# Performance work log

Hardware: AMD Instinct MI355X
Metric: run time of the kernel (lower is better)

The kernel has to match this reference:

```python
import jax, jax.numpy as jnp
import numpy as np

MARGIN = 0.1
B, D, NUM_CLASSES = 512, 128, 64


def _pairwise_sq_dist(e):
    # squared pairwise distances with clamp + off-diagonal masking,
    # matching pairwise_distance_torch (NOTE: no sqrt in the original).
    sq = jnp.sum(e * e, axis=-1)                       # [B]
    d = sq[:, None] + sq[None, :] - 2.0 * (e @ e.T)    # [B, B]
    d = jnp.maximum(d, 0.0)
    d = d * (d > 0.0).astype(jnp.float32)              # error_mask step
    n = e.shape[0]
    return d * (1.0 - jnp.eye(n, dtype=jnp.float32))   # zero diagonal


def setup_inputs() -> dict:
    key = jax.random.key(0)
    k1, k2 = jax.random.split(key)
    emb = jax.random.normal(k1, (B, D), dtype=jnp.float32)
    emb = emb / jnp.linalg.norm(emb, axis=-1, keepdims=True)  # l2-normalized per docstring
    labels = jax.random.randint(k2, (B,), 0, NUM_CLASSES, dtype=jnp.int64 if jax.config.read('jax_enable_x64') else jnp.int32)
    return {"embeddings": emb, "labels": labels}


def reference(embeddings, labels):
    e = embeddings.astype(jnp.float32)
    pdist = _pairwise_sq_dist(e)                       # [B, B]
    n = labels.shape[0]
    adj = labels[:, None] == labels[None, :]           # [B, B] bool
    adj_not = ~adj

    # Tiled mining tensor, expressed as [i, j, k] where j = anchor,
    # k = negative candidate, i = positive candidate.
    # mask3[i, j, k] = (label[j] != label[k]) & (d(j,k) > d(j,i))
    mask3 = (adj_not[None, :, :] & (pdist[None, :, :] > pdist.T[:, :, None])).astype(jnp.float32)

    # masked min over negatives k (min-over-mask via row-max shift trick, as in torch code)
    row_max = jnp.max(pdist, axis=1, keepdims=True)    # [B, 1] per anchor j
    mm = jnp.min((pdist[None, :, :] - row_max[None, :, :]) * mask3, axis=2) + row_max[None, :, 0]  # [i, j]
    negatives_outside = mm.T                           # [anchor j, positive i]
    mask_final = (jnp.sum(mask3, axis=2) > 0.0).T      # [j, i]: semi-hard negative exists

    # fallback: hardest (largest) negative per anchor
    row_min = jnp.min(pdist, axis=1, keepdims=True)    # [B, 1]
    anf = adj_not.astype(jnp.float32)
    masked_max = jnp.max((pdist - row_min) * anf, axis=1, keepdims=True) + row_min  # [B, 1]
    negatives_inside = jnp.broadcast_to(masked_max, (n, n))

    semi_hard_negatives = jnp.where(mask_final, negatives_outside, negatives_inside)
    loss_mat = MARGIN + pdist - semi_hard_negatives

    mask_positives = adj.astype(jnp.float32) - jnp.eye(n, dtype=jnp.float32)
    num_positives = jnp.sum(mask_positives)
    triplet_loss = jnp.sum(jnp.maximum(loss_mat * mask_positives, 0.0)) / num_positives
    return triplet_loss.astype(embeddings.dtype)
```

## Files before the change

kernel.cpp:

```cpp
#include <hip/hip_runtime.h>
#include <cfloat>


constexpr int   BN       = 512;
constexpr int   DD       = 128;
constexpr float MARGIN_F = 0.1f;
constexpr int   NBLK     = BN / 2;

template <int CTRL>
__device__ inline float dppAdd(float v) {
    int x = __builtin_amdgcn_update_dpp(__float_as_int(v), __float_as_int(v),
                                        CTRL, 0xF, 0xF, false);
    return v + __int_as_float(x);
}
template <int CTRL>
__device__ inline float dppMin(float v) {
    int x = __builtin_amdgcn_update_dpp(__float_as_int(v), __float_as_int(v),
                                        CTRL, 0xF, 0xF, false);
    return fminf(v, __int_as_float(x));
}
template <int CTRL>
__device__ inline float dppMax(float v) {
    int x = __builtin_amdgcn_update_dpp(__float_as_int(v), __float_as_int(v),
                                        CTRL, 0xF, 0xF, false);
    return fmaxf(v, __int_as_float(x));
}
constexpr int DPP_XOR1 = 0xB1;
constexpr int DPP_XOR2 = 0x4E;
constexpr int DPP_ROR4 = 0x124;
constexpr int DPP_ROR8 = 0x128;

__device__ inline float waveMin64(float v) {
    v = dppMin<DPP_XOR1>(v);
    v = dppMin<DPP_XOR2>(v);
    v = dppMin<DPP_ROR4>(v);
    v = dppMin<DPP_ROR8>(v);
    v = fminf(v, __shfl_xor(v, 16, 64));
    v = fminf(v, __shfl_xor(v, 32, 64));
    return v;
}
__device__ inline float waveMax64(float v) {
    v = dppMax<DPP_XOR1>(v);
    v = dppMax<DPP_XOR2>(v);
    v = dppMax<DPP_ROR4>(v);
    v = dppMax<DPP_ROR8>(v);
    v = fmaxf(v, __shfl_xor(v, 16, 64));
    v = fmaxf(v, __shfl_xor(v, 32, 64));
    return v;
}

__global__ __launch_bounds__(512) void triplet_anchor(
    const float* __restrict__ emb, const int* __restrict__ labels,
    float* __restrict__ loss_part, int* __restrict__ cnt_part)
{
    __shared__ __align__(16) float ej0[DD];
    __shared__ __align__(16) float ej1[DD];
    __shared__ __align__(16) float dist0[BN];
    __shared__ __align__(16) float dist1[BN];
    __shared__ float wsum8[8];

    const int t    = threadIdx.x;
    const int w    = t >> 6;
    const int lane = t & 63;
    const int sub  = t & 3;
    const int a0   = blockIdx.x * 2;
    const int a1   = a0 + 1;

    if (t < DD)          ej0[t]      = emb[(size_t)a0 * DD + t];
    else if (t < 2 * DD) ej1[t - DD] = emb[(size_t)a1 * DD + (t - DD)];
    __syncthreads();

    float4 e0q[8], e1q[8];
    {
        const float4* ej0v = reinterpret_cast<const float4*>(ej0);
        const float4* ej1v = reinterpret_cast<const float4*>(ej1);
#pragma unroll
        for (int qq = 0; qq < 8; ++qq) {
            e0q[qq] = ej0v[qq * 4 + sub];
            e1q[qq] = ej1v[qq * 4 + sub];
        }
    }

    const int rbase = t >> 2;
#pragma unroll 2
    for (int pass = 0; pass < 4; ++pass) {
        const int r = pass * 128 + rbase;
        const float4* rowv = reinterpret_cast<const float4*>(emb + (size_t)r * DD);
        float d0 = 0.f, d1 = 0.f;
#pragma unroll
        for (int qq = 0; qq < 8; ++qq) {
            const float4 b = rowv[qq * 4 + sub];
            const float4 A = e0q[qq], C = e1q[qq];
            d0 += A.x * b.x + A.y * b.y + A.z * b.z + A.w * b.w;
            d1 += C.x * b.x + C.y * b.y + C.z * b.z + C.w * b.w;
        }
        d0 = dppAdd<DPP_XOR1>(d0);
        d0 = dppAdd<DPP_XOR2>(d0);
        d1 = dppAdd<DPP_XOR1>(d1);
        d1 = dppAdd<DPP_XOR2>(d1);
        if (sub == 0) {
            const float dd = fmaxf(2.f - 2.f * d0, 0.f);
            dist0[r] = (r == a0) ? 0.f : dd;
        } else if (sub == 1) {
            const float dd = fmaxf(2.f - 2.f * d1, 0.f);
            dist1[r] = (r == a1) ? 0.f : dd;
        }
    }
    __syncthreads();

    const int    A     = (w < 4) ? a0 : a1;
    const int    wi    = w & 3;
    const float* distA = (w < 4) ? dist0 : dist1;

    const float4* dv  = reinterpret_cast<const float4*>(distA) + lane * 2;
    const float4  dA4 = dv[0], dB4 = dv[1];
    const int4*   lv  = reinterpret_cast<const int4*>(labels) + lane * 2;
    const int4    lA4 = lv[0], lB4 = lv[1];
    const float ddv[8] = {dA4.x, dA4.y, dA4.z, dA4.w, dB4.x, dB4.y, dB4.z, dB4.w};
    const int   llv[8] = {lA4.x, lA4.y, lA4.z, lA4.w, lB4.x, lB4.y, lB4.z, lB4.w};
    const int   labA   = labels[A];

    float dn[8];
    float nmax = 0.f;
#pragma unroll
    for (int q = 0; q < 8; ++q) {
        const bool neg = (llv[q] != labA);
        dn[q] = neg ? ddv[q] : FLT_MAX;
        nmax  = neg ? fmaxf(nmax, ddv[q]) : nmax;
    }
    const float neg_inside = waveMax64(nmax);

    int   npos = 0;
    int   p    = 0;
    float wsum = 0.f;
#pragma unroll
    for (int q = 0; q < 8; ++q) {
        unsigned long long m = __ballot((llv[q] == labA) && (lane * 8 + q != A));
        npos += __popcll(m);
        while (m) {
            const int src = __ffsll((long long)m) - 1;
            m &= m - 1;
            if ((p & 3) == wi) {
                const float dpos = __shfl(ddv[q], src, 64);
                float mn = FLT_MAX;
#pragma unroll
                for (int qq = 0; qq < 8; ++qq)
                    mn = fminf(mn, (dn[qq] > dpos) ? dn[qq] : FLT_MAX);
                mn = waveMin64(mn);
                const float shn = (mn < FLT_MAX) ? mn : neg_inside;
                wsum += fmaxf(MARGIN_F + dpos - shn, 0.f);
            }
            ++p;
        }
    }
    if (lane == 0) wsum8[w] = wsum;
    if (lane == 1 && (w == 0 || w == 4)) cnt_part[A] = npos;
    __syncthreads();
    if (t == 0) loss_part[a0] = (wsum8[0] + wsum8[1]) + (wsum8[2] + wsum8[3]);
    if (t == 1) loss_part[a1] = (wsum8[4] + wsum8[5]) + (wsum8[6] + wsum8[7]);
}

__global__ __launch_bounds__(64) void triplet_finalize(
    const float* __restrict__ loss_part, const int* __restrict__ cnt_part,
    float* __restrict__ out)
{
    const int t = threadIdx.x;
    const float4* lp = reinterpret_cast<const float4*>(loss_part);
    const int4*   cp = reinterpret_cast<const int4*>(cnt_part);
    const float4 s0 = lp[t], s1 = lp[t + 64];
    const int4   c0 = cp[t], c1 = cp[t + 64];
    float s = ((s0.x + s0.y) + (s0.z + s0.w)) + ((s1.x + s1.y) + (s1.z + s1.w));
    int   c = (c0.x + c0.y + c0.z + c0.w) + (c1.x + c1.y + c1.z + c1.w);
#pragma unroll
    for (int o = 1; o < 64; o <<= 1) {
        s += __shfl_xor(s, o, 64);
        c += __shfl_xor(c, o, 64);
    }
    if (t == 0) out[0] = s / (float)c;
}

extern "C" void kernel_launch(void* const* d_in, const int* in_sizes, int n_in,
                              void* d_out, int out_size, void* d_ws, size_t ws_size,
                              hipStream_t stream)
{
    const float* emb    = (const float*)d_in[0];
    const int*   labels = (const int*)d_in[1];
    float*       out    = (float*)d_out;

    float* loss_part = (float*)d_ws;
    int*   cnt_part  = (int*)((char*)d_ws + BN * sizeof(float));

    triplet_anchor<<<NBLK, 512, 0, stream>>>(emb, labels, loss_part, cnt_part);
    triplet_finalize<<<1, 64, 0, stream>>>(loss_part, cnt_part, out);
}
```

Before: 13.35 us.

## Double block size to 1024 threads, split positives across 8 waves per anchor

Launches 1024 threads per block, so the distance pass over the 512 rows takes 2 iterations instead of 4, and 8 waves per anchor share the positive-candidate loop instead of 4. Anchor embeddings are now loaded straight from global memory into registers, which removes the shared staging and one barrier. The positive distance is broadcast with readlane instead of a shuffle. Larger blocks may lower occupancy and add more block-level reduction work, which could offset the shorter per-wave work.

```diff
diff --git a/kernel.cpp b/kernel.cpp
--- a/kernel.cpp
+++ b/kernel.cpp
@@ -49,15 +49,13 @@
     return v;
 }
 
-__global__ __launch_bounds__(512) void triplet_anchor(
+__global__ __launch_bounds__(1024) void triplet_anchor(
     const float* __restrict__ emb, const int* __restrict__ labels,
     float* __restrict__ loss_part, int* __restrict__ cnt_part)
 {
-    __shared__ __align__(16) float ej0[DD];
-    __shared__ __align__(16) float ej1[DD];
     __shared__ __align__(16) float dist0[BN];
     __shared__ __align__(16) float dist1[BN];
-    __shared__ float wsum8[8];
+    __shared__ float wsum16[16];
 
     const int t    = threadIdx.x;
     const int w    = t >> 6;
@@ -66,25 +64,21 @@
     const int a0   = blockIdx.x * 2;
     const int a1   = a0 + 1;
 
-    if (t < DD)          ej0[t]      = emb[(size_t)a0 * DD + t];
-    else if (t < 2 * DD) ej1[t - DD] = emb[(size_t)a1 * DD + (t - DD)];
-    __syncthreads();
-
     float4 e0q[8], e1q[8];
     {
-        const float4* ej0v = reinterpret_cast<const float4*>(ej0);
-        const float4* ej1v = reinterpret_cast<const float4*>(ej1);
+        const float4* e0v = reinterpret_cast<const float4*>(emb + (size_t)a0 * DD);
+        const float4* e1v = reinterpret_cast<const float4*>(emb + (size_t)a1 * DD);
 #pragma unroll
         for (int qq = 0; qq < 8; ++qq) {
-            e0q[qq] = ej0v[qq * 4 + sub];
-            e1q[qq] = ej1v[qq * 4 + sub];
+            e0q[qq] = e0v[qq * 4 + sub];
+            e1q[qq] = e1v[qq * 4 + sub];
         }
     }
 
     const int rbase = t >> 2;
-#pragma unroll 2
-    for (int pass = 0; pass < 4; ++pass) {
-        const int r = pass * 128 + rbase;
+#pragma unroll
+    for (int pass = 0; pass < 2; ++pass) {
+        const int r = pass * 256 + rbase;
         const float4* rowv = reinterpret_cast<const float4*>(emb + (size_t)r * DD);
         float d0 = 0.f, d1 = 0.f;
 #pragma unroll
@@ -108,9 +102,9 @@
     }
     __syncthreads();
 
-    const int    A     = (w < 4) ? a0 : a1;
-    const int    wi    = w & 3;
-    const float* distA = (w < 4) ? dist0 : dist1;
+    const int    A     = (w < 8) ? a0 : a1;
+    const int    wi    = w & 7;
+    const float* distA = (w < 8) ? dist0 : dist1;
 
     const float4* dv  = reinterpret_cast<const float4*>(distA) + lane * 2;
     const float4  dA4 = dv[0], dB4 = dv[1];
@@ -140,8 +134,9 @@
         while (m) {
             const int src = __ffsll((long long)m) - 1;
             m &= m - 1;
-            if ((p & 3) == wi) {
-                const float dpos = __shfl(ddv[q], src, 64);
+            if ((p & 7) == wi) {
+                const float dpos = __int_as_float(
+                    __builtin_amdgcn_readlane(__float_as_int(ddv[q]), src));
                 float mn = FLT_MAX;
 #pragma unroll
                 for (int qq = 0; qq < 8; ++qq)
@@ -153,11 +148,15 @@
             ++p;
         }
     }
-    if (lane == 0) wsum8[w] = wsum;
-    if (lane == 1 && (w == 0 || w == 4)) cnt_part[A] = npos;
+    if (lane == 0) wsum16[w] = wsum;
+    if (lane == 1 && (w == 0 || w == 8)) cnt_part[A] = npos;
     __syncthreads();
-    if (t == 0) loss_part[a0] = (wsum8[0] + wsum8[1]) + (wsum8[2] + wsum8[3]);
-    if (t == 1) loss_part[a1] = (wsum8[4] + wsum8[5]) + (wsum8[6] + wsum8[7]);
+    if (t == 0)
+        loss_part[a0] = ((wsum16[0] + wsum16[1]) + (wsum16[2] + wsum16[3]))
+                      + ((wsum16[4] + wsum16[5]) + (wsum16[6] + wsum16[7]));
+    if (t == 1)
+        loss_part[a1] = ((wsum16[8] + wsum16[9]) + (wsum16[10] + wsum16[11]))
+                      + ((wsum16[12] + wsum16[13]) + (wsum16[14] + wsum16[15]));
 }
 
 __global__ __launch_bounds__(64) void triplet_finalize(
@@ -190,6 +189,6 @@
     float* loss_part = (float*)d_ws;
     int*   cnt_part  = (int*)((char*)d_ws + BN * sizeof(float));
 
-    triplet_anchor<<<NBLK, 512, 0, stream>>>(emb, labels, loss_part, cnt_part);
+    triplet_anchor<<<NBLK, 1024, 0, stream>>>(emb, labels, loss_part, cnt_part);
     triplet_finalize<<<1, 64, 0, stream>>>(loss_part, cnt_part, out);
 }
```

After: 14.35 us. +7.5%, slower.

## Split into tiled Gram-distance kernel and per-wave mining kernel

Applied to the files above, without the earlier changes.

Adds a three-kernel path that first computes the full 512x512 distance matrix with a shared-memory tiled Gram kernel and writes it to workspace. A mining kernel then gives each wave its own anchor and processes every positive without the round-robin split across waves, using readlane-based scalar reductions in place of cross-lane shuffles. A 64-entry finalize kernel follows. This is meant to remove the redundant per-anchor reads of the embedding matrix. In exchange it adds an extra launch, a 1 MB global round trip for the distance matrix, and a serial positive loop per wave. The old path is kept as a fallback when the workspace is too small.

```diff
diff --git a/kernel.cpp b/kernel.cpp
--- a/kernel.cpp
+++ b/kernel.cpp
@@ -30,6 +30,25 @@
 constexpr int DPP_ROR4 = 0x124;
 constexpr int DPP_ROR8 = 0x128;
 
+__device__ inline float rdlane(float v, int l) {
+    return __int_as_float(__builtin_amdgcn_readlane(__float_as_int(v), l));
+}
+__device__ inline float waveMinU(float v) {
+    v = dppMin<DPP_XOR1>(v);
+    v = dppMin<DPP_XOR2>(v);
+    v = dppMin<DPP_ROR4>(v);
+    v = dppMin<DPP_ROR8>(v);
+    return fminf(fminf(rdlane(v, 0), rdlane(v, 16)),
+                 fminf(rdlane(v, 32), rdlane(v, 48)));
+}
+__device__ inline float waveMaxU(float v) {
+    v = dppMax<DPP_XOR1>(v);
+    v = dppMax<DPP_XOR2>(v);
+    v = dppMax<DPP_ROR4>(v);
+    v = dppMax<DPP_ROR8>(v);
+    return fmaxf(fmaxf(rdlane(v, 0), rdlane(v, 16)),
+                 fmaxf(rdlane(v, 32), rdlane(v, 48)));
+}
 __device__ inline float waveMin64(float v) {
     v = dppMin<DPP_XOR1>(v);
     v = dppMin<DPP_XOR2>(v);
@@ -47,6 +66,133 @@
     v = fmaxf(v, __shfl_xor(v, 16, 64));
     v = fmaxf(v, __shfl_xor(v, 32, 64));
     return v;
+}
+
+__global__ __launch_bounds__(256) void gram_k(
+    const float* __restrict__ emb, float* __restrict__ dist)
+{
+    __shared__ __align__(16) float rows[32][132];
+    __shared__ __align__(16) float cols[32][132];
+
+    const int t  = threadIdx.x;
+    const int ti = blockIdx.x >> 4;
+    const int tj = blockIdx.x & 15;
+
+    const float4* embv = reinterpret_cast<const float4*>(emb);
+#pragma unroll
+    for (int i = 0; i < 4; ++i) {
+        const int gi = t + i * 256;
+        const int r  = gi >> 5;
+        const int q  = gi & 31;
+        *reinterpret_cast<float4*>(&rows[r][q * 4]) = embv[(ti * 32 + r) * 32 + q];
+        *reinterpret_cast<float4*>(&cols[r][q * 4]) = embv[(tj * 32 + r) * 32 + q];
+    }
+    __syncthreads();
+
+    const int c  = t & 31;
+    const int rq = t >> 5;
+    float acc0 = 0.f, acc1 = 0.f, acc2 = 0.f, acc3 = 0.f;
+    const float* colp = &cols[c][0];
+    const float* r0p  = &rows[rq * 4 + 0][0];
+    const float* r1p  = &rows[rq * 4 + 1][0];
+    const float* r2p  = &rows[rq * 4 + 2][0];
+    const float* r3p  = &rows[rq * 4 + 3][0];
+#pragma unroll
+    for (int q = 0; q < 32; ++q) {
+        const float4 b  = *reinterpret_cast<const float4*>(colp + q * 4);
+        const float4 a0 = *reinterpret_cast<const float4*>(r0p + q * 4);
+        const float4 a1 = *reinterpret_cast<const float4*>(r1p + q * 4);
+        const float4 a2 = *reinterpret_cast<const float4*>(r2p + q * 4);
+        const float4 a3 = *reinterpret_cast<const float4*>(r3p + q * 4);
+        acc0 += a0.x * b.x + a0.y * b.y + a0.z * b.z + a0.w * b.w;
+        acc1 += a1.x * b.x + a1.y * b.y + a1.z * b.z + a1.w * b.w;
+        acc2 += a2.x * b.x + a2.y * b.y + a2.z * b.z + a2.w * b.w;
+        acc3 += a3.x * b.x + a3.y * b.y + a3.z * b.z + a3.w * b.w;
+    }
+    const int cg = tj * 32 + c;
+    const float acc[4] = {acc0, acc1, acc2, acc3};
+#pragma unroll
+    for (int rr = 0; rr < 4; ++rr) {
+        const int r = ti * 32 + rq * 4 + rr;
+        float d = fmaxf(2.f - 2.f * acc[rr], 0.f);
+        if (r == cg) d = 0.f;
+        dist[r * BN + cg] = d;
+    }
+}
+
+__global__ __launch_bounds__(512) void mine_k(
+    const float* __restrict__ dist, const int* __restrict__ labels,
+    float* __restrict__ loss_blk, int* __restrict__ cnt_blk)
+{
+    __shared__ float ws8[8];
+    __shared__ int   wc8[8];
+
+    const int t    = threadIdx.x;
+    const int w    = t >> 6;
+    const int lane = t & 63;
+    const int A    = blockIdx.x * 8 + w;
+
+    const float4* dv  = reinterpret_cast<const float4*>(dist + (size_t)A * BN)
+                        + lane * 2;
+    const float4  dA4 = dv[0], dB4 = dv[1];
+    const int4*   lv  = reinterpret_cast<const int4*>(labels) + lane * 2;
+    const int4    lA4 = lv[0], lB4 = lv[1];
+    const float ddv[8] = {dA4.x, dA4.y, dA4.z, dA4.w, dB4.x, dB4.y, dB4.z, dB4.w};
+    const int   llv[8] = {lA4.x, lA4.y, lA4.z, lA4.w, lB4.x, lB4.y, lB4.z, lB4.w};
+    const int   labA   = labels[A];
+
+    float dn[8];
+    float nmax = 0.f;
+#pragma unroll
+    for (int q = 0; q < 8; ++q) {
+        const bool neg = (llv[q] != labA);
+        dn[q] = neg ? ddv[q] : FLT_MAX;
+        nmax  = neg ? fmaxf(nmax, ddv[q]) : nmax;
+    }
+    const float neg_inside = waveMaxU(nmax);
+
+    int   npos = 0;
+    float wsum = 0.f;
+#pragma unroll
+    for (int q = 0; q < 8; ++q) {
+        unsigned long long m = __ballot((llv[q] == labA) && (lane * 8 + q != A));
+        npos += __popcll(m);
+        while (m) {
+            const int src = __ffsll((long long)m) - 1;
+            m &= m - 1;
+            const float dpos = rdlane(ddv[q], src);
+            float mn = FLT_MAX;
+#pragma unroll
+            for (int qq = 0; qq < 8; ++qq)
+                mn = fminf(mn, (dn[qq] > dpos) ? dn[qq] : FLT_MAX);
+            mn = waveMinU(mn);
+            const float shn = (mn < FLT_MAX) ? mn : neg_inside;
+            wsum += fmaxf(MARGIN_F + dpos - shn, 0.f);
+        }
+    }
+    if (lane == 0) { ws8[w] = wsum; wc8[w] = npos; }
+    __syncthreads();
+    if (t == 0) {
+        loss_blk[blockIdx.x] = ((ws8[0] + ws8[1]) + (ws8[2] + ws8[3]))
+                             + ((ws8[4] + ws8[5]) + (ws8[6] + ws8[7]));
+        cnt_blk[blockIdx.x]  = ((wc8[0] + wc8[1]) + (wc8[2] + wc8[3]))
+                             + ((wc8[4] + wc8[5]) + (wc8[6] + wc8[7]));
+    }
+}
+
+__global__ __launch_bounds__(64) void fin64_k(
+    const float* __restrict__ loss_blk, const int* __restrict__ cnt_blk,
+    float* __restrict__ out)
+{
+    const int t = threadIdx.x;
+    float s = loss_blk[t];
+    int   c = cnt_blk[t];
+#pragma unroll
+    for (int o = 1; o < 64; o <<= 1) {
+        s += __shfl_xor(s, o, 64);
+        c += __shfl_xor(c, o, 64);
+    }
+    if (t == 0) out[0] = s / (float)c;
 }
 
 __global__ __launch_bounds__(512) void triplet_anchor(
@@ -187,9 +333,19 @@
     const int*   labels = (const int*)d_in[1];
     float*       out    = (float*)d_out;
 
-    float* loss_part = (float*)d_ws;
-    int*   cnt_part  = (int*)((char*)d_ws + BN * sizeof(float));
-
-    triplet_anchor<<<NBLK, 512, 0, stream>>>(emb, labels, loss_part, cnt_part);
-    triplet_finalize<<<1, 64, 0, stream>>>(loss_part, cnt_part, out);
-}
+    const size_t need = (size_t)BN * BN * sizeof(float) + 64 * (sizeof(float) + sizeof(int));
+    if (ws_size >= need) {
+        float* dist     = (float*)d_ws;
+        float* loss_blk = (float*)((char*)d_ws + (size_t)BN * BN * sizeof(float));
+        int*   cnt_blk  = (int*)((char*)loss_blk + 64 * sizeof(float));
+
+        gram_k<<<256, 256, 0, stream>>>(emb, dist);
+        mine_k<<<64, 512, 0, stream>>>(dist, labels, loss_blk, cnt_blk);
+        fin64_k<<<1, 64, 0, stream>>>(loss_blk, cnt_blk, out);
+    } else {
+        float* loss_part = (float*)d_ws;
+        int*   cnt_part  = (int*)((char*)d_ws + BN * sizeof(float));
+        triplet_anchor<<<NBLK, 512, 0, stream>>>(emb, labels, loss_part, cnt_part);
+        triplet_finalize<<<1, 64, 0, stream>>>(loss_part, cnt_part, out);
+    }
+}
```

After: 15.91 us. 19.2% more time.
